# Kernel optimization log

Hardware: AMD Instinct MI355X
Metric: run time of the kernel (lower is better)

## Reference

```python
import jax, jax.numpy as jnp
import numpy as np


def setup_inputs() -> dict:
    key = jax.random.key(0)
    ks = jax.random.split(key, 8)
    B, C, H, W = 4, 256, 64, 64
    C8 = C // 8
    s = 0.05
    return {
        "x": jax.random.normal(ks[0], (B, C, H, W), jnp.float32),
        "wq": jax.random.normal(ks[1], (C8, C), jnp.float32) * s,
        "bq": jax.random.normal(ks[2], (C8,), jnp.float32) * s,
        "wk": jax.random.normal(ks[3], (C8, C), jnp.float32) * s,
        "bk": jax.random.normal(ks[4], (C8,), jnp.float32) * s,
        "wv": jax.random.normal(ks[5], (C, C), jnp.float32) * s,
        "bv": jax.random.normal(ks[6], (C,), jnp.float32) * s,
        "gamma": jax.random.uniform(ks[7], (1,), jnp.float32),
    }


def reference(x, wq, bq, wk, bk, wv, bv, gamma):
    B, C, H, W = x.shape
    N = H * W
    xf = x.reshape(B, C, N)  # flatten spatial: [B, C, N]
    # 1x1 convs are channel-wise matmuls
    q = jnp.einsum("dc,bcn->bnd", wq, xf) + bq[None, None, :]  # [B, N, C/8]
    k = jnp.einsum("dc,bcn->bdn", wk, xf) + bk[None, :, None]  # [B, C/8, N]
    v = jnp.einsum("dc,bcn->bdn", wv, xf) + bv[None, :, None]  # [B, C, N]
    energy = jnp.einsum("bnd,bdm->bnm", q, k)  # [B, N, N]
    attention = jax.nn.softmax(energy, axis=-1)
    # out = value @ attention^T  -> [B, C, N]
    out = jnp.einsum("bcm,bnm->bcn", v, attention)
    out = out.reshape(B, C, H, W)
    return gamma[0] * out + x
```

## Files before the change

kernel.cpp:

```cpp
#include <hip/hip_runtime.h>
#include <hip/hip_bf16.h>
#include <stdint.h>

#define B_ 4
#define C_ 256
#define N_ 4096
#define D_ 32
#define KT 256

typedef __bf16 bf16_t;
typedef __bf16 bf16x4_t __attribute__((ext_vector_type(4)));
typedef __bf16 bf16x8_t __attribute__((ext_vector_type(8)));
typedef float  f32x4    __attribute__((ext_vector_type(4)));

__device__ __forceinline__ void gld_lds16(const void* g, void* l) {
  __builtin_amdgcn_global_load_lds((__attribute__((address_space(1))) void*)g,
                                   (__attribute__((address_space(3))) void*)l, 16, 0, 0);
}

__global__ __launch_bounds__(256) void cast_kernel(
    const float* __restrict__ x,
    const float* __restrict__ wq, const float* __restrict__ wk,
    const float* __restrict__ wv,
    bf16_t* __restrict__ xbT, bf16_t* __restrict__ Wb)
{
  const int bid = blockIdx.x;
  const int t = threadIdx.x;
  if (bid >= 1024) {
    const int gr = bid - 1024;
    float v;
    if (gr < 32)      v = wq[gr * C_ + t];
    else if (gr < 64) v = wk[(gr - 32) * C_ + t];
    else              v = wv[(gr - 64) * C_ + t];
    Wb[gr * C_ + t] = (bf16_t)v;
    return;
  }
  __shared__ float xs[64][65];
  const int n0 = (bid & 63) * 64;
  const int c0 = ((bid >> 6) & 3) * 64;
  const int b  = bid >> 8;

  const int lr = t >> 4;
  const int lc = (t & 15) * 4;
#pragma unroll
  for (int i = 0; i < 4; ++i) {
    const f32x4 v = *(const f32x4*)(x + ((size_t)(b * C_ + c0 + lr + i * 16)) * N_ + n0 + lc);
    xs[lr + i * 16][lc + 0] = v[0];
    xs[lr + i * 16][lc + 1] = v[1];
    xs[lr + i * 16][lc + 2] = v[2];
    xs[lr + i * 16][lc + 3] = v[3];
  }
  __syncthreads();
  const int nr = t >> 2;
  const int cb = (t & 3) * 16;
  bf16_t tmp[16];
#pragma unroll
  for (int j = 0; j < 16; ++j) tmp[j] = (bf16_t)xs[cb + j][nr];
  bf16_t* dst = xbT + ((size_t)(b * N_ + n0 + nr)) * C_ + c0 + cb;
  *(bf16x8_t*)dst       = *(bf16x8_t*)&tmp[0];
  *(bf16x8_t*)(dst + 8) = *(bf16x8_t*)&tmp[8];
}

__global__ __launch_bounds__(256) void proj_kernel(
    const bf16_t* __restrict__ Wb, const bf16_t* __restrict__ xbT,
    const float* __restrict__ bq, const float* __restrict__ bk,
    const float* __restrict__ bv,
    bf16_t* __restrict__ Qh, bf16_t* __restrict__ Kh, bf16_t* __restrict__ Vh)
{
  const int bi = blockIdx.x;
  const int b  = bi & 3;
  const int n0 = (bi >> 2) * 64;
  const int t = threadIdx.x, w = t >> 6, lane = t & 63;
  const int l4 = lane >> 4, lm = lane & 15;

  const f32x4 z4 = {0.f, 0.f, 0.f, 0.f};
  f32x4 acc[5][4];
#pragma unroll
  for (int rt = 0; rt < 5; ++rt)
#pragma unroll
    for (int ct = 0; ct < 4; ++ct) acc[rt][ct] = z4;

#pragma unroll 1
  for (int k0 = 0; k0 < C_; k0 += 64) {
    bf16x8_t af[5][2], bfr[4][2];
#pragma unroll
    for (int rt = 0; rt < 5; ++rt)
#pragma unroll
      for (int kc = 0; kc < 2; ++kc)
        af[rt][kc] = *(const bf16x8_t*)(Wb + (size_t)(w * 80 + rt * 16 + lm) * C_ + k0 + kc * 32 + l4 * 8);
#pragma unroll
    for (int ct = 0; ct < 4; ++ct)
#pragma unroll
      for (int kc = 0; kc < 2; ++kc)
        bfr[ct][kc] = *(const bf16x8_t*)(xbT + ((size_t)(b * N_ + n0 + ct * 16 + lm)) * C_ + k0 + kc * 32 + l4 * 8);
#pragma unroll
    for (int rt = 0; rt < 5; ++rt)
#pragma unroll
      for (int ct = 0; ct < 4; ++ct)
#pragma unroll
        for (int kc = 0; kc < 2; ++kc)
          acc[rt][ct] = __builtin_amdgcn_mfma_f32_16x16x32_bf16(af[rt][kc], bfr[ct][kc], acc[rt][ct], 0, 0, 0);
  }

#pragma unroll
  for (int rt = 0; rt < 5; ++rt)
#pragma unroll
    for (int r = 0; r < 4; ++r) {
      const int gr = w * 80 + rt * 16 + 4 * l4 + r;
      const float bias = (gr < 32) ? bq[gr] : (gr < 64) ? bk[gr - 32] : bv[gr - 64];
#pragma unroll
      for (int ct = 0; ct < 4; ++ct) {
        const int n = n0 + ct * 16 + lm;
        float v = acc[rt][ct][r] + bias;
        if (gr < 32) {
          v *= 1.44269504088896f;
          Qh[((size_t)(b * N_ + n)) * D_ + gr] = (bf16_t)v;
        } else if (gr < 64) {
          Kh[((size_t)(b * N_ + n)) * D_ + (gr - 32)] = (bf16_t)v;
        } else {
          Vh[((size_t)(b * C_ + (gr - 64))) * N_ + n] = (bf16_t)v;
        }
      }
    }
}

__global__ __launch_bounds__(512, 2) void attn_kernel(
    const bf16_t* __restrict__ Qh, const bf16_t* __restrict__ Kh,
    const bf16_t* __restrict__ Vh, const float* __restrict__ x,
    const float* __restrict__ gamma, float* __restrict__ out)
{
  __shared__ __align__(16) bf16_t Vt[3][C_][64];
  __shared__ __align__(16) bf16_t Pl[2][32][KT];
  __shared__ __align__(16) float  PMx[2][64][4];
  __shared__ __align__(16) float  PSx[2][64][4];

  const int bi = blockIdx.x;
  const int xcd = bi & 7, slot = bi >> 3;
  const int b  = xcd >> 1;
  const int q0 = ((xcd & 1) * 32 + slot) * 64;

  const int t = threadIdx.x, wid = t >> 6, lane = t & 63;
  const int l4 = lane >> 4, lm = lane & 15;
  const int rh = wid & 1, cg = wid >> 1;
  const int pswz = (lm & 7) << 3;

  const f32x4 z4 = {0.f, 0.f, 0.f, 0.f};

  const int vr  = lane >> 3;
  const int msw = ((lane & 7) ^ vr) << 3;
  const bf16_t* vsrc[4];
#pragma unroll
  for (int u = 0; u < 4; ++u)
    vsrc[u] = Vh + ((size_t)(b * C_ + 32 * wid + 8 * u + vr)) * N_ + msw;

#pragma unroll
  for (int u = 0; u < 4; ++u) gld_lds16(vsrc[u], &Vt[0][32 * wid + 8 * u][0]);
#pragma unroll
  for (int u = 0; u < 4; ++u) gld_lds16(vsrc[u] + 64, &Vt[1][32 * wid + 8 * u][0]);

  const bf16_t* kbase = Kh + ((size_t)(b * N_ + cg * 64 + lm)) * D_ + l4 * 8;

  bf16x8_t qf[2];
#pragma unroll
  for (int rt2 = 0; rt2 < 2; ++rt2)
    qf[rt2] = *(const bf16x8_t*)(Qh + ((size_t)(b * N_ + q0 + rh * 32 + rt2 * 16 + lm)) * D_ + l4 * 8);

  f32x4 acc[2][4];
#pragma unroll
  for (int rt2 = 0; rt2 < 2; ++rt2)
#pragma unroll
    for (int ct = 0; ct < 4; ++ct) acc[rt2][ct] = z4;
  float m_run[2] = {-1e30f, -1e30f}, l_run[2] = {0.f, 0.f};

  int bufc = 0;
#pragma unroll 1
  for (int it = 0; it < N_ / KT; ++it) {
    bf16x8_t kf[4];
#pragma unroll
    for (int mt = 0; mt < 4; ++mt)
      kf[mt] = *(const bf16x8_t*)(kbase + (size_t)(it * KT + mt * 16) * D_);

    f32x4 S[2][4];
#pragma unroll
    for (int rt2 = 0; rt2 < 2; ++rt2)
#pragma unroll
      for (int mt = 0; mt < 4; ++mt)
        S[rt2][mt] = __builtin_amdgcn_mfma_f32_16x16x32_bf16(kf[mt], qf[rt2], z4, 0, 0, 0);

    float pmx[2];
#pragma unroll
    for (int rt2 = 0; rt2 < 2; ++rt2) {
      float a0 = fmaxf(fmaxf(S[rt2][0][0], S[rt2][0][1]), fmaxf(S[rt2][0][2], S[rt2][0][3]));
      float a1 = fmaxf(fmaxf(S[rt2][1][0], S[rt2][1][1]), fmaxf(S[rt2][1][2], S[rt2][1][3]));
      float a2 = fmaxf(fmaxf(S[rt2][2][0], S[rt2][2][1]), fmaxf(S[rt2][2][2], S[rt2][2][3]));
      float a3 = fmaxf(fmaxf(S[rt2][3][0], S[rt2][3][1]), fmaxf(S[rt2][3][2], S[rt2][3][3]));
      float v = fmaxf(fmaxf(a0, a1), fmaxf(a2, a3));
      v = fmaxf(v, __shfl_xor(v, 16));
      v = fmaxf(v, __shfl_xor(v, 32));
      pmx[rt2] = v;
    }
    if (lane < 32) PMx[rh][lane][cg] = (lane < 16) ? pmx[0] : pmx[1];
    asm volatile("s_waitcnt lgkmcnt(0)" ::: "memory");
    __builtin_amdgcn_s_barrier();

    float sc[2], nm[2]; int chg[2];
#pragma unroll
    for (int rt2 = 0; rt2 < 2; ++rt2) {
      const f32x4 pv = *(const f32x4*)&PMx[rh][rt2 * 16 + lm][0];
      const float tm = fmaxf(fmaxf(pv[0], pv[1]), fmaxf(pv[2], pv[3]));
      const float mo = m_run[rt2];
      nm[rt2]  = fmaxf(mo, tm);
      chg[rt2] = tm > mo;
      sc[rt2]  = __builtin_amdgcn_exp2f(mo - nm[rt2]);
      m_run[rt2] = nm[rt2];
    }

    float psx[2];
#pragma unroll
    for (int rt2 = 0; rt2 < 2; ++rt2) {
      float s = 0.f;
      const int prow = rt2 * 16 + lm;
#pragma unroll
      for (int mt = 0; mt < 4; ++mt) {
        const float p0 = __builtin_amdgcn_exp2f(S[rt2][mt][0] - nm[rt2]);
        const float p1 = __builtin_amdgcn_exp2f(S[rt2][mt][1] - nm[rt2]);
        const float p2 = __builtin_amdgcn_exp2f(S[rt2][mt][2] - nm[rt2]);
        const float p3 = __builtin_amdgcn_exp2f(S[rt2][mt][3] - nm[rt2]);
        s += (p0 + p1) + (p2 + p3);
        bf16x4_t w4 = {(bf16_t)p0, (bf16_t)p1, (bf16_t)p2, (bf16_t)p3};
        *(bf16x4_t*)&Pl[rh][prow][(cg * 64 + 16 * mt + 4 * l4) ^ pswz] = w4;
      }
      s += __shfl_xor(s, 16);
      s += __shfl_xor(s, 32);
      psx[rt2] = s;
    }
    if (lane < 32) PSx[rh][lane][cg] = (lane < 16) ? psx[0] : psx[1];

    if (__any(chg[0] || chg[1])) {
#pragma unroll
      for (int rt2 = 0; rt2 < 2; ++rt2)
#pragma unroll
        for (int ct = 0; ct < 4; ++ct) acc[rt2][ct] *= sc[rt2];
    }
    asm volatile("s_waitcnt lgkmcnt(0)" ::: "memory");
    __builtin_amdgcn_s_barrier();

#pragma unroll
    for (int rt2 = 0; rt2 < 2; ++rt2) {
      const f32x4 sv = *(const f32x4*)&PSx[rh][rt2 * 16 + lm][0];
      l_run[rt2] = l_run[rt2] * sc[rt2] + ((sv[0] + sv[1]) + (sv[2] + sv[3]));
    }

#pragma unroll
    for (int s4 = 0; s4 < 4; ++s4) {
      if (s4 == 0)
        asm volatile("s_waitcnt vmcnt(4) lgkmcnt(0)" ::: "memory");
      else
        asm volatile("s_waitcnt vmcnt(4)" ::: "memory");
      __builtin_amdgcn_s_barrier();

      const int knx = (it * KT + (s4 + 2) * 64) & (N_ - 1);
      const int bst = (bufc < 1) ? bufc + 2 : bufc - 1;
#pragma unroll
      for (int u = 0; u < 4; ++u)
        gld_lds16(vsrc[u] + knx, &Vt[bst][32 * wid + 8 * u][0]);

      bf16x8_t pa[2][2];
#pragma unroll
      for (int rt2 = 0; rt2 < 2; ++rt2)
#pragma unroll
        for (int kc = 0; kc < 2; ++kc)
          pa[rt2][kc] = *(const bf16x8_t*)&Pl[rh][rt2 * 16 + lm][(s4 * 64 + kc * 32 + 8 * l4) ^ pswz];
#pragma unroll
      for (int ct = 0; ct < 4; ++ct) {
#pragma unroll
        for (int kc = 0; kc < 2; ++kc) {
          const bf16x8_t vf = *(const bf16x8_t*)&Vt[bufc][cg * 64 + ct * 16 + lm][(kc * 32 + 8 * l4) ^ pswz];
#pragma unroll
          for (int rt2 = 0; rt2 < 2; ++rt2)
            acc[rt2][ct] = __builtin_amdgcn_mfma_f32_16x16x32_bf16(vf, pa[rt2][kc], acc[rt2][ct], 0, 0, 0);
        }
      }
      bufc = (bufc == 2) ? 0 : bufc + 1;
    }
  }

  const float g = gamma[0];
  const int n = q0 + rh * 32 + lm;
#pragma unroll
  for (int rt2 = 0; rt2 < 2; ++rt2) {
    const float inv = 1.f / l_run[rt2];
#pragma unroll
    for (int ct = 0; ct < 4; ++ct) {
#pragma unroll
      for (int r = 0; r < 4; ++r) {
        const int c = cg * 64 + ct * 16 + 4 * l4 + r;
        const size_t idx = ((size_t)(b * C_ + c)) * N_ + n + rt2 * 16;
        out[idx] = g * (acc[rt2][ct][r] * inv) + x[idx];
      }
    }
  }
}

extern "C" void kernel_launch(void* const* d_in, const int* in_sizes, int n_in,
                              void* d_out, int out_size, void* d_ws, size_t ws_size,
                              hipStream_t stream) {
  const float* x     = (const float*)d_in[0];
  const float* wq    = (const float*)d_in[1];
  const float* bq    = (const float*)d_in[2];
  const float* wk    = (const float*)d_in[3];
  const float* bk    = (const float*)d_in[4];
  const float* wv    = (const float*)d_in[5];
  const float* bv    = (const float*)d_in[6];
  const float* gamma = (const float*)d_in[7];
  float* out = (float*)d_out;

  bf16_t* Qh  = (bf16_t*)d_ws;
  bf16_t* Kh  = Qh + (size_t)B_ * N_ * D_;
  bf16_t* Vh  = Kh + (size_t)B_ * N_ * D_;
  bf16_t* Wb  = Vh + (size_t)B_ * C_ * N_;
  bf16_t* xbT = Wb + (size_t)320 * C_;

  cast_kernel<<<1344, 256, 0, stream>>>(x, wq, wk, wv, xbT, Wb);
  proj_kernel<<<256, 256, 0, stream>>>(Wb, xbT, bq, bk, bv, Qh, Kh, Vh);
  attn_kernel<<<256, 512, 0, stream>>>(Qh, Kh, Vh, x, gamma, out);
}
```

Measured before the change: 114.6 us.

## Repartition attention work per wave and stream V directly into registers

Each of the 8 waves now covers all 64 query rows and owns a 32-channel slice of V and a 32-key slice of each KT tile, instead of splitting rows in halves and channels in quarters. V fragments are loaded straight from global memory into double-buffered registers rather than staged in LDS through a 3-stage global_load_lds ring, which removes the per-subtile barriers. K for the next tile is also prefetched into registers. The trade is uncoalesced, per-lane 16-byte global loads of V and higher register pressure, in exchange for less LDS traffic and synchronisation.

```diff
diff --git a/kernel.cpp b/kernel.cpp
--- a/kernel.cpp
+++ b/kernel.cpp
@@ -12,11 +12,6 @@
 typedef __bf16 bf16x4_t __attribute__((ext_vector_type(4)));
 typedef __bf16 bf16x8_t __attribute__((ext_vector_type(8)));
 typedef float  f32x4    __attribute__((ext_vector_type(4)));
-
-__device__ __forceinline__ void gld_lds16(const void* g, void* l) {
-  __builtin_amdgcn_global_load_lds((__attribute__((address_space(1))) void*)g,
-                                   (__attribute__((address_space(3))) void*)l, 16, 0, 0);
-}
 
 __global__ __launch_bounds__(256) void cast_kernel(
     const float* __restrict__ x,
@@ -129,174 +124,192 @@
     const bf16_t* __restrict__ Vh, const float* __restrict__ x,
     const float* __restrict__ gamma, float* __restrict__ out)
 {
-  __shared__ __align__(16) bf16_t Vt[3][C_][64];
-  __shared__ __align__(16) bf16_t Pl[2][32][KT];
-  __shared__ __align__(16) float  PMx[2][64][4];
-  __shared__ __align__(16) float  PSx[2][64][4];
+  __shared__ __align__(16) bf16_t Pl[64][KT];
+  __shared__ __align__(16) float  PMx[64][8];
+  __shared__ __align__(16) float  PSx[64][8];
 
   const int bi = blockIdx.x;
   const int xcd = bi & 7, slot = bi >> 3;
   const int b  = xcd >> 1;
   const int q0 = ((xcd & 1) * 32 + slot) * 64;
 
-  const int t = threadIdx.x, wid = t >> 6, lane = t & 63;
+  const int t = threadIdx.x, w = t >> 6, lane = t & 63;
   const int l4 = lane >> 4, lm = lane & 15;
-  const int rh = wid & 1, cg = wid >> 1;
-  const int pswz = (lm & 7) << 3;
+  const int swz = (lm & 7) << 3;
 
   const f32x4 z4 = {0.f, 0.f, 0.f, 0.f};
 
-  const int vr  = lane >> 3;
-  const int msw = ((lane & 7) ^ vr) << 3;
-  const bf16_t* vsrc[4];
-#pragma unroll
-  for (int u = 0; u < 4; ++u)
-    vsrc[u] = Vh + ((size_t)(b * C_ + 32 * wid + 8 * u + vr)) * N_ + msw;
-
-#pragma unroll
-  for (int u = 0; u < 4; ++u) gld_lds16(vsrc[u], &Vt[0][32 * wid + 8 * u][0]);
-#pragma unroll
-  for (int u = 0; u < 4; ++u) gld_lds16(vsrc[u] + 64, &Vt[1][32 * wid + 8 * u][0]);
-
-  const bf16_t* kbase = Kh + ((size_t)(b * N_ + cg * 64 + lm)) * D_ + l4 * 8;
-
-  bf16x8_t qf[2];
-#pragma unroll
-  for (int rt2 = 0; rt2 < 2; ++rt2)
-    qf[rt2] = *(const bf16x8_t*)(Qh + ((size_t)(b * N_ + q0 + rh * 32 + rt2 * 16 + lm)) * D_ + l4 * 8);
+  bf16x8_t qf[4];
+#pragma unroll
+  for (int rt = 0; rt < 4; ++rt)
+    qf[rt] = *(const bf16x8_t*)(Qh + ((size_t)(b * N_ + q0 + rt * 16 + lm)) * D_ + l4 * 8);
+
+  const bf16_t* kbase = Kh + ((size_t)(b * N_ + w * 32 + lm)) * D_ + l4 * 8;
+  const bf16_t* vbase = Vh + ((size_t)(b * C_ + w * 32 + lm)) * N_ + l4 * 8;
 
   f32x4 acc[2][4];
 #pragma unroll
-  for (int rt2 = 0; rt2 < 2; ++rt2)
-#pragma unroll
-    for (int ct = 0; ct < 4; ++ct) acc[rt2][ct] = z4;
-  float m_run[2] = {-1e30f, -1e30f}, l_run[2] = {0.f, 0.f};
-
-  int bufc = 0;
+  for (int ct = 0; ct < 2; ++ct)
+#pragma unroll
+    for (int rt = 0; rt < 4; ++rt) acc[ct][rt] = z4;
+  float m_run[4] = {-1e30f, -1e30f, -1e30f, -1e30f};
+  float l_run[4] = {0.f, 0.f, 0.f, 0.f};
+
+  bf16x8_t kf[2], kn[2];
+#pragma unroll
+  for (int mt = 0; mt < 2; ++mt)
+    kf[mt] = *(const bf16x8_t*)(kbase + (size_t)(mt * 16) * D_);
+  bf16x8_t vf0[2][2], vf1[2][2];
+#pragma unroll
+  for (int ct = 0; ct < 2; ++ct)
+#pragma unroll
+    for (int kc = 0; kc < 2; ++kc) {
+      vf0[ct][kc] = *(const bf16x8_t*)(vbase + (size_t)(ct * 16) * N_ + kc * 32);
+      vf1[ct][kc] = *(const bf16x8_t*)(vbase + (size_t)(ct * 16) * N_ + 64 + kc * 32);
+    }
+
 #pragma unroll 1
   for (int it = 0; it < N_ / KT; ++it) {
-    bf16x8_t kf[4];
-#pragma unroll
-    for (int mt = 0; mt < 4; ++mt)
-      kf[mt] = *(const bf16x8_t*)(kbase + (size_t)(it * KT + mt * 16) * D_);
-
-    f32x4 S[2][4];
-#pragma unroll
-    for (int rt2 = 0; rt2 < 2; ++rt2)
-#pragma unroll
-      for (int mt = 0; mt < 4; ++mt)
-        S[rt2][mt] = __builtin_amdgcn_mfma_f32_16x16x32_bf16(kf[mt], qf[rt2], z4, 0, 0, 0);
-
-    float pmx[2];
-#pragma unroll
-    for (int rt2 = 0; rt2 < 2; ++rt2) {
-      float a0 = fmaxf(fmaxf(S[rt2][0][0], S[rt2][0][1]), fmaxf(S[rt2][0][2], S[rt2][0][3]));
-      float a1 = fmaxf(fmaxf(S[rt2][1][0], S[rt2][1][1]), fmaxf(S[rt2][1][2], S[rt2][1][3]));
-      float a2 = fmaxf(fmaxf(S[rt2][2][0], S[rt2][2][1]), fmaxf(S[rt2][2][2], S[rt2][2][3]));
-      float a3 = fmaxf(fmaxf(S[rt2][3][0], S[rt2][3][1]), fmaxf(S[rt2][3][2], S[rt2][3][3]));
-      float v = fmaxf(fmaxf(a0, a1), fmaxf(a2, a3));
+    f32x4 S[4][2];
+#pragma unroll
+    for (int rt = 0; rt < 4; ++rt)
+#pragma unroll
+      for (int mt = 0; mt < 2; ++mt)
+        S[rt][mt] = __builtin_amdgcn_mfma_f32_16x16x32_bf16(kf[mt], qf[rt], z4, 0, 0, 0);
+
+    float pmx[4];
+#pragma unroll
+    for (int rt = 0; rt < 4; ++rt) {
+      float a0 = fmaxf(fmaxf(S[rt][0][0], S[rt][0][1]), fmaxf(S[rt][0][2], S[rt][0][3]));
+      float a1 = fmaxf(fmaxf(S[rt][1][0], S[rt][1][1]), fmaxf(S[rt][1][2], S[rt][1][3]));
+      float v = fmaxf(a0, a1);
       v = fmaxf(v, __shfl_xor(v, 16));
       v = fmaxf(v, __shfl_xor(v, 32));
-      pmx[rt2] = v;
-    }
-    if (lane < 32) PMx[rh][lane][cg] = (lane < 16) ? pmx[0] : pmx[1];
+      pmx[rt] = v;
+    }
+    {
+      const float pw = (l4 == 0) ? pmx[0] : (l4 == 1) ? pmx[1] : (l4 == 2) ? pmx[2] : pmx[3];
+      PMx[l4 * 16 + lm][w] = pw;
+    }
     asm volatile("s_waitcnt lgkmcnt(0)" ::: "memory");
     __builtin_amdgcn_s_barrier();
 
-    float sc[2], nm[2]; int chg[2];
-#pragma unroll
-    for (int rt2 = 0; rt2 < 2; ++rt2) {
-      const f32x4 pv = *(const f32x4*)&PMx[rh][rt2 * 16 + lm][0];
-      const float tm = fmaxf(fmaxf(pv[0], pv[1]), fmaxf(pv[2], pv[3]));
-      const float mo = m_run[rt2];
-      nm[rt2]  = fmaxf(mo, tm);
-      chg[rt2] = tm > mo;
-      sc[rt2]  = __builtin_amdgcn_exp2f(mo - nm[rt2]);
-      m_run[rt2] = nm[rt2];
-    }
-
-    float psx[2];
-#pragma unroll
-    for (int rt2 = 0; rt2 < 2; ++rt2) {
+    float nm[4], sc[4]; int chg = 0;
+#pragma unroll
+    for (int rt = 0; rt < 4; ++rt) {
+      const f32x4 p0 = *(const f32x4*)&PMx[rt * 16 + lm][0];
+      const f32x4 p1 = *(const f32x4*)&PMx[rt * 16 + lm][4];
+      const float tm = fmaxf(fmaxf(fmaxf(p0[0], p0[1]), fmaxf(p0[2], p0[3])),
+                             fmaxf(fmaxf(p1[0], p1[1]), fmaxf(p1[2], p1[3])));
+      const float mo = m_run[rt];
+      nm[rt] = fmaxf(mo, tm);
+      chg |= (tm > mo);
+      sc[rt] = __builtin_amdgcn_exp2f(mo - nm[rt]);
+      m_run[rt] = nm[rt];
+    }
+
+    float psx[4];
+#pragma unroll
+    for (int rt = 0; rt < 4; ++rt) {
       float s = 0.f;
-      const int prow = rt2 * 16 + lm;
-#pragma unroll
-      for (int mt = 0; mt < 4; ++mt) {
-        const float p0 = __builtin_amdgcn_exp2f(S[rt2][mt][0] - nm[rt2]);
-        const float p1 = __builtin_amdgcn_exp2f(S[rt2][mt][1] - nm[rt2]);
-        const float p2 = __builtin_amdgcn_exp2f(S[rt2][mt][2] - nm[rt2]);
-        const float p3 = __builtin_amdgcn_exp2f(S[rt2][mt][3] - nm[rt2]);
+      const int prow = rt * 16 + lm;
+#pragma unroll
+      for (int mt = 0; mt < 2; ++mt) {
+        const float p0 = __builtin_amdgcn_exp2f(S[rt][mt][0] - nm[rt]);
+        const float p1 = __builtin_amdgcn_exp2f(S[rt][mt][1] - nm[rt]);
+        const float p2 = __builtin_amdgcn_exp2f(S[rt][mt][2] - nm[rt]);
+        const float p3 = __builtin_amdgcn_exp2f(S[rt][mt][3] - nm[rt]);
         s += (p0 + p1) + (p2 + p3);
         bf16x4_t w4 = {(bf16_t)p0, (bf16_t)p1, (bf16_t)p2, (bf16_t)p3};
-        *(bf16x4_t*)&Pl[rh][prow][(cg * 64 + 16 * mt + 4 * l4) ^ pswz] = w4;
+        *(bf16x4_t*)&Pl[prow][(w * 32 + mt * 16 + 4 * l4) ^ swz] = w4;
       }
       s += __shfl_xor(s, 16);
       s += __shfl_xor(s, 32);
-      psx[rt2] = s;
-    }
-    if (lane < 32) PSx[rh][lane][cg] = (lane < 16) ? psx[0] : psx[1];
-
-    if (__any(chg[0] || chg[1])) {
-#pragma unroll
-      for (int rt2 = 0; rt2 < 2; ++rt2)
-#pragma unroll
-        for (int ct = 0; ct < 4; ++ct) acc[rt2][ct] *= sc[rt2];
-    }
+      psx[rt] = s;
+    }
+    {
+      const float pw = (l4 == 0) ? psx[0] : (l4 == 1) ? psx[1] : (l4 == 2) ? psx[2] : psx[3];
+      PSx[l4 * 16 + lm][w] = pw;
+    }
+
+    if (__any(chg)) {
+#pragma unroll
+      for (int ct = 0; ct < 2; ++ct)
+#pragma unroll
+        for (int rt = 0; rt < 4; ++rt) acc[ct][rt] *= sc[rt];
+    }
+
+    const int k0n = ((it + 1) * KT) & (N_ - 1);
+#pragma unroll
+    for (int mt = 0; mt < 2; ++mt)
+      kn[mt] = *(const bf16x8_t*)(kbase + (size_t)(k0n + mt * 16) * D_);
+
     asm volatile("s_waitcnt lgkmcnt(0)" ::: "memory");
     __builtin_amdgcn_s_barrier();
 
 #pragma unroll
-    for (int rt2 = 0; rt2 < 2; ++rt2) {
-      const f32x4 sv = *(const f32x4*)&PSx[rh][rt2 * 16 + lm][0];
-      l_run[rt2] = l_run[rt2] * sc[rt2] + ((sv[0] + sv[1]) + (sv[2] + sv[3]));
+    for (int rt = 0; rt < 4; ++rt) {
+      const f32x4 s0 = *(const f32x4*)&PSx[rt * 16 + lm][0];
+      const f32x4 s1 = *(const f32x4*)&PSx[rt * 16 + lm][4];
+      l_run[rt] = l_run[rt] * sc[rt] +
+                  (((s0[0] + s0[1]) + (s0[2] + s0[3])) + ((s1[0] + s1[1]) + (s1[2] + s1[3])));
     }
 
 #pragma unroll
     for (int s4 = 0; s4 < 4; ++s4) {
-      if (s4 == 0)
-        asm volatile("s_waitcnt vmcnt(4) lgkmcnt(0)" ::: "memory");
-      else
-        asm volatile("s_waitcnt vmcnt(4)" ::: "memory");
-      __builtin_amdgcn_s_barrier();
-
-      const int knx = (it * KT + (s4 + 2) * 64) & (N_ - 1);
-      const int bst = (bufc < 1) ? bufc + 2 : bufc - 1;
-#pragma unroll
-      for (int u = 0; u < 4; ++u)
-        gld_lds16(vsrc[u] + knx, &Vt[bst][32 * wid + 8 * u][0]);
-
-      bf16x8_t pa[2][2];
-#pragma unroll
-      for (int rt2 = 0; rt2 < 2; ++rt2)
+      bf16x8_t pa[4][2];
+#pragma unroll
+      for (int rt = 0; rt < 4; ++rt)
 #pragma unroll
         for (int kc = 0; kc < 2; ++kc)
-          pa[rt2][kc] = *(const bf16x8_t*)&Pl[rh][rt2 * 16 + lm][(s4 * 64 + kc * 32 + 8 * l4) ^ pswz];
-#pragma unroll
-      for (int ct = 0; ct < 4; ++ct) {
-#pragma unroll
-        for (int kc = 0; kc < 2; ++kc) {
-          const bf16x8_t vf = *(const bf16x8_t*)&Vt[bufc][cg * 64 + ct * 16 + lm][(kc * 32 + 8 * l4) ^ pswz];
-#pragma unroll
-          for (int rt2 = 0; rt2 < 2; ++rt2)
-            acc[rt2][ct] = __builtin_amdgcn_mfma_f32_16x16x32_bf16(vf, pa[rt2][kc], acc[rt2][ct], 0, 0, 0);
-        }
+          pa[rt][kc] = *(const bf16x8_t*)&Pl[rt * 16 + lm][(s4 * 64 + kc * 32 + l4 * 8) ^ swz];
+      if ((s4 & 1) == 0) {
+#pragma unroll
+        for (int ct = 0; ct < 2; ++ct)
+#pragma unroll
+          for (int kc = 0; kc < 2; ++kc)
+#pragma unroll
+            for (int rt = 0; rt < 4; ++rt)
+              acc[ct][rt] = __builtin_amdgcn_mfma_f32_16x16x32_bf16(vf0[ct][kc], pa[rt][kc], acc[ct][rt], 0, 0, 0);
+        const int knx = (it * KT + (s4 + 2) * 64) & (N_ - 1);
+#pragma unroll
+        for (int ct = 0; ct < 2; ++ct)
+#pragma unroll
+          for (int kc = 0; kc < 2; ++kc)
+            vf0[ct][kc] = *(const bf16x8_t*)(vbase + (size_t)(ct * 16) * N_ + knx + kc * 32);
+      } else {
+#pragma unroll
+        for (int ct = 0; ct < 2; ++ct)
+#pragma unroll
+          for (int kc = 0; kc < 2; ++kc)
+#pragma unroll
+            for (int rt = 0; rt < 4; ++rt)
+              acc[ct][rt] = __builtin_amdgcn_mfma_f32_16x16x32_bf16(vf1[ct][kc], pa[rt][kc], acc[ct][rt], 0, 0, 0);
+        const int knx = (it * KT + (s4 + 2) * 64) & (N_ - 1);
+#pragma unroll
+        for (int ct = 0; ct < 2; ++ct)
+#pragma unroll
+          for (int kc = 0; kc < 2; ++kc)
+            vf1[ct][kc] = *(const bf16x8_t*)(vbase + (size_t)(ct * 16) * N_ + knx + kc * 32);
       }
-      bufc = (bufc == 2) ? 0 : bufc + 1;
-    }
+    }
+
+#pragma unroll
+    for (int mt = 0; mt < 2; ++mt) kf[mt] = kn[mt];
   }
 
   const float g = gamma[0];
-  const int n = q0 + rh * 32 + lm;
-#pragma unroll
-  for (int rt2 = 0; rt2 < 2; ++rt2) {
-    const float inv = 1.f / l_run[rt2];
-#pragma unroll
-    for (int ct = 0; ct < 4; ++ct) {
+#pragma unroll
+  for (int rt = 0; rt < 4; ++rt) {
+    const float inv = 1.f / l_run[rt];
+    const int n = q0 + rt * 16 + lm;
+#pragma unroll
+    for (int ct = 0; ct < 2; ++ct) {
 #pragma unroll
       for (int r = 0; r < 4; ++r) {
-        const int c = cg * 64 + ct * 16 + 4 * l4 + r;
-        const size_t idx = ((size_t)(b * C_ + c)) * N_ + n + rt2 * 16;
-        out[idx] = g * (acc[rt2][ct][r] * inv) + x[idx];
+        const int c = w * 32 + ct * 16 + 4 * l4 + r;
+        const size_t idx = ((size_t)(b * C_ + c)) * N_ + n;
+        out[idx] = g * (acc[ct][rt][r] * inv) + x[idx];
       }
     }
   }
```

Result: faster. 104.5 us (-8.8%).
